# Kernel optimization log

Hardware: AMD Instinct MI355X
Metric: run time of the kernel (lower is better)

Reference implementation:

```python
import jax, jax.numpy as jnp
import numpy as np
import math

E = 768      # embed_size
H = 12       # heads
D = E // H   # head_dim = 64
MAXLEN = 512
N = 8        # batch
L = 512      # seq_len (q_len == k_len)


def _sinusoid_table():
    # (2*MAXLEN-1, E) sinusoidal table, sin at even dims, cos at odd dims
    pos = jnp.arange(2 * MAXLEN - 1, dtype=jnp.float32)[:, None]
    div = jnp.exp(jnp.arange(0, E, 2, dtype=jnp.float32) * (-math.log(10000.0) / E))
    ang = pos * div  # (2M-1, E/2)
    return jnp.stack([jnp.sin(ang), jnp.cos(ang)], axis=-1).reshape(2 * MAXLEN - 1, E)


def setup_inputs() -> dict:
    key = jax.random.key(0)
    ks = jax.random.split(key, 16)
    sc = 0.02
    return {
        "values": jax.random.normal(ks[0], (N, L, E), jnp.float32),
        "keys": jax.random.normal(ks[1], (N, L, E), jnp.float32),
        "query": jax.random.normal(ks[2], (N, L, E), jnp.float32),
        "Wq": jax.random.normal(ks[3], (E, E), jnp.float32) * sc,
        "bq": jax.random.normal(ks[4], (E,), jnp.float32) * sc,
        "Wk": jax.random.normal(ks[5], (E, E), jnp.float32) * sc,
        "bk": jax.random.normal(ks[6], (E,), jnp.float32) * sc,
        "Wv": jax.random.normal(ks[7], (E, E), jnp.float32) * sc,
        "bv": jax.random.normal(ks[8], (E,), jnp.float32) * sc,
        "Wo": jax.random.normal(ks[9], (E, E), jnp.float32) * sc,
        "bo": jax.random.normal(ks[10], (E,), jnp.float32) * sc,
        "Wpos": jax.random.normal(ks[11], (E, E), jnp.float32) * sc,
        "bpos": jax.random.normal(ks[12], (E,), jnp.float32) * sc,
        "r_w_bias": jax.random.normal(ks[13], (H, D), jnp.float32),
        "r_r_bias": jax.random.normal(ks[14], (H, D), jnp.float32),
    }


def _rel_shift(x):
    # Faithful to the torch code: pad one row on q dim, shape-preserving view,
    # drop first row -> identity as written.
    xp = jnp.pad(x, ((0, 0), (0, 0), (1, 0), (0, 0)))
    return xp[:, :, 1:, :]


def reference(values, keys, query, Wq, bq, Wk, bk, Wv, bv, Wo, bo, Wpos, bpos, r_w_bias, r_r_bias):
    pe = _sinusoid_table()  # (2M-1, E)
    r = jnp.arange(L)
    idx = jnp.clip(r[:, None] - r[None, :] + (MAXLEN - 1), 0, 2 * MAXLEN - 2)  # (L, L)
    rel = pe[idx] @ Wpos + bpos                       # (L, L, E)
    rel = rel.reshape(L, L, H, D).transpose(2, 0, 1, 3)  # (H, L, L, D)

    q = (query @ Wq + bq).reshape(N, L, H, D)
    k = (keys @ Wk + bk).reshape(N, L, H, D)
    v = (values @ Wv + bv).reshape(N, L, H, D)

    ac = jnp.einsum('nqhd,nkhd->nhqk', q + r_w_bias[None, None], k)
    bd = jnp.einsum('nqhd,hqkd->nhqk', q + r_r_bias[None, None], rel)
    bd = _rel_shift(bd)

    scores = (ac + bd) / math.sqrt(D)
    attn = jax.nn.softmax(scores, axis=-1)
    out = jnp.einsum('nhqk,nkhd->nqhd', attn, v).reshape(N, L, E)
    return out @ Wo + bo
```

## Files before the change

kernel.cpp:

```cpp
#include <hip/hip_runtime.h>

typedef unsigned short u16;
typedef unsigned int u32;
typedef __bf16 bf16x8 __attribute__((ext_vector_type(8)));
typedef float f32x4 __attribute__((ext_vector_type(4)));

#define EMB 768
#define NH 12
#define HD 64
#define SEQ 512
#define NB 8
#define NLROWS 4096
#define PEROWS 1024

__device__ __forceinline__ float b2f(u16 u) {
    return __uint_as_float(((u32)u) << 16);
}
__device__ __forceinline__ u16 f2b(float f) {
    u32 x = __float_as_uint(f);
    u32 r = x + 0x7fffu + ((x >> 16) & 1u);
    return (u16)(r >> 16);
}
__device__ __forceinline__ u32 pack2(float a, float b) {
    return (u32)f2b(a) | ((u32)f2b(b) << 16);
}
__device__ __forceinline__ void gl_lds16(const u16* g, u16* l) {
    __builtin_amdgcn_global_load_lds((const __attribute__((address_space(1))) u32*)g,
                                     (__attribute__((address_space(3))) u32*)l, 16, 0, 0);
}

__global__ __launch_bounds__(256) void prep(
        const float* __restrict__ Wq, const float* __restrict__ Wk, const float* __restrict__ Wv,
        const float* __restrict__ Wo, const float* __restrict__ Wpos,
        u16* __restrict__ Wt, u16* __restrict__ pe,
        const float* __restrict__ q, const float* __restrict__ k, const float* __restrict__ v,
        u16* __restrict__ qc, u16* __restrict__ kc, u16* __restrict__ vc) {
    __shared__ u16 tile[32][33];
    int b = blockIdx.x;
    int tid = threadIdx.x;
    if (b < 2880) {
        int m = b / 576, r = b % 576;
        const float* src = (m == 0) ? Wq : (m == 1) ? Wk : (m == 2) ? Wv : (m == 3) ? Wo : Wpos;
        u16* dst = Wt + (size_t)m * EMB * EMB;
        int bx = (r % 24) * 32, by = (r / 24) * 32;
        int tx = tid & 31, ty = tid >> 5;
#pragma unroll
        for (int i = 0; i < 32; i += 8)
            tile[ty + i][tx] = f2b(src[(size_t)(by + ty + i) * EMB + bx + tx]);
        __syncthreads();
#pragma unroll
        for (int i = 0; i < 32; i += 8)
            dst[(size_t)(bx + ty + i) * EMB + by + tx] = tile[tx][ty + i];
    } else if (b < 3904) {
        int pos = b - 2880;
        int p2 = pos > 1022 ? 1022 : pos;
#pragma unroll
        for (int j = 0; j < 3; j++) {
            int col = tid + j * 256;
            int i = col >> 1;
            float ang = (float)p2 * __expf(-0.023985261384f * (float)i);
            float val = (col & 1) ? __cosf(ang) : __sinf(ang);
            pe[(size_t)pos * EMB + col] = f2b(val);
        }
    } else {
        int idx = b - 3904;
        int w = idx / 1536, bx = idx % 1536;
        const float* s = (w == 0) ? q : (w == 1) ? k : v;
        u16* d = (w == 0) ? qc : (w == 1) ? kc : vc;
        size_t i = ((size_t)bx * 256 + tid) * 8;
        float4 f0 = *(const float4*)(s + i);
        float4 f1 = *(const float4*)(s + i + 4);
        uint4 o;
        o.x = pack2(f0.x, f0.y); o.y = pack2(f0.z, f0.w);
        o.z = pack2(f1.x, f1.y); o.w = pack2(f1.z, f1.w);
        *(uint4*)(d + i) = o;
    }
}

template <int BM, int BN, int NZ, bool OUTF32>
__global__ __launch_bounds__(256, 4) void gemm_k(
        const u16* A0, const u16* A1, const u16* A2, const u16* A3,
        const u16* W0, const u16* W1, const u16* W2, const u16* W3,
        const float* f0, const float* f1, const float* f2, const float* f3,
        void* C0, void* C1, void* C2, void* C3) {
    constexpr int RT = BM / 32;
    constexpr int CT = BN / 32;
    __shared__ __align__(16) u16 As[BM * 64];
    __shared__ __align__(16) u16 Bs[BN * 64];
    int z = (NZ > 1) ? blockIdx.z : 0;
    if (NZ > 1 && z == 3 && blockIdx.x >= PEROWS / BM) return;
    const u16* A = (z == 0) ? A0 : (z == 1) ? A1 : (z == 2) ? A2 : A3;
    const u16* Bt = (z == 0) ? W0 : (z == 1) ? W1 : (z == 2) ? W2 : W3;
    const float* bias = (z == 0) ? f0 : (z == 1) ? f1 : (z == 2) ? f2 : f3;
    void* Cv = (z == 0) ? C0 : (z == 1) ? C1 : (z == 2) ? C2 : C3;
    bool vtout = (NZ > 1) && (z == 2);

    int tid = threadIdx.x;
    int wave = tid >> 6, lane = tid & 63;
    int lrow = lane & 15, lq = lane >> 4;
    int lr8 = lane >> 3, lb = lane & 7;
    int m0 = blockIdx.x * BM, n0 = blockIdx.y * BN;
    int wr = (wave >> 1) * (BM / 2), wc = (wave & 1) * (BN / 2);
    const u16* Abase = A + (size_t)m0 * EMB + (size_t)(lb ^ lr8) * 8;
    const u16* Bbase = Bt + (size_t)n0 * EMB + (size_t)(lb ^ lr8) * 8;
    f32x4 acc[RT][CT] = {};

    for (int k0 = 0; k0 < EMB; k0 += 64) {
        __syncthreads();
#pragma unroll
        for (int j = 0; j < BM / 32; j++) {
            int row = j * 32 + wave * 8 + lr8;
            gl_lds16(Abase + (size_t)row * EMB + k0, &As[(j * 32 + wave * 8) * 64]);
        }
#pragma unroll
        for (int j = 0; j < BN / 32; j++) {
            int row = j * 32 + wave * 8 + lr8;
            gl_lds16(Bbase + (size_t)row * EMB + k0, &Bs[(j * 32 + wave * 8) * 64]);
        }
        __syncthreads();
#pragma unroll
        for (int ks = 0; ks < 2; ks++) {
            int pb = (ks * 4 + lq) ^ (lrow & 7);
            bf16x8 bfr[CT];
#pragma unroll
            for (int ct = 0; ct < CT; ct++)
                bfr[ct] = *(const bf16x8*)&Bs[(wc + ct * 16 + lrow) * 64 + pb * 8];
#pragma unroll
            for (int rt = 0; rt < RT; rt++) {
                bf16x8 afr = *(const bf16x8*)&As[(wr + rt * 16 + lrow) * 64 + pb * 8];
#pragma unroll
                for (int ct = 0; ct < CT; ct++)
                    acc[rt][ct] = __builtin_amdgcn_mfma_f32_16x16x32_bf16(afr, bfr[ct], acc[rt][ct], 0, 0, 0);
            }
        }
    }
#pragma unroll
    for (int rt = 0; rt < RT; rt++) {
#pragma unroll
        for (int ct = 0; ct < CT; ct++) {
            int col = n0 + wc + ct * 16 + lrow;
            float bvv = bias[col];
            int mrow = m0 + wr + rt * 16 + lq * 4;
            if (vtout) {
                int nb = mrow >> 9, kvl = mrow & 511;
                int hh = col >> 6, dl = col & 63;
                ushort4 pk;
                pk.x = f2b(acc[rt][ct][0] + bvv);
                pk.y = f2b(acc[rt][ct][1] + bvv);
                pk.z = f2b(acc[rt][ct][2] + bvv);
                pk.w = f2b(acc[rt][ct][3] + bvv);
                *(ushort4*)((u16*)Cv + (((size_t)(nb * NH + hh) * HD + dl) << 9) + kvl) = pk;
            } else if (OUTF32) {
#pragma unroll
                for (int r = 0; r < 4; r++)
                    ((float*)Cv)[(size_t)(mrow + r) * EMB + col] = acc[rt][ct][r] + bvv;
            } else {
#pragma unroll
                for (int r = 0; r < 4; r++)
                    ((u16*)Cv)[(size_t)(mrow + r) * EMB + col] = f2b(acc[rt][ct][r] + bvv);
            }
        }
    }
}

__global__ __launch_bounds__(256, 3) void attn_rpe(
        const u16* __restrict__ Qb, const u16* __restrict__ Kb, const u16* __restrict__ Vtg,
        const u16* __restrict__ Rb, const float* __restrict__ rwb, const float* __restrict__ rrb,
        u16* __restrict__ Ctx) {
    __shared__ __align__(16) u16 Ks[64 * 64];
    __shared__ __align__(16) u16 Vt[64 * 64];
    __shared__ __align__(16) u16 Rs[128 * 64];
    __shared__ __align__(16) u16 PsPb[4 * 1664];

    int q0 = blockIdx.x * 64;
    int h = blockIdx.y;
    int n = blockIdx.z;
    int tid = threadIdx.x;
    int wave = tid >> 6, lane = tid & 63;
    int lrow = lane & 15, lq = lane >> 4;
    int lr8 = lane >> 3, lb = lane & 7;
    int swz = (lb ^ lr8) * 8;
    u16* psd = &PsPb[wave * 1664];

    bf16x8 aw[2], ar[2];
    {
        const u16* qrow = Qb + ((size_t)(n * SEQ + q0 + wave * 16 + lrow)) * EMB + h * HD;
#pragma unroll
        for (int ks = 0; ks < 2; ks++) {
            int c = ks * 32 + lq * 8;
            uint4 qv = *(const uint4*)(qrow + c);
            float4 w0 = *(const float4*)(rwb + h * HD + c);
            float4 w1 = *(const float4*)(rwb + h * HD + c + 4);
            float4 r0 = *(const float4*)(rrb + h * HD + c);
            float4 r1 = *(const float4*)(rrb + h * HD + c + 4);
            union { uint4 u; u16 s[8]; } qu; qu.u = qv;
            union { uint4 u; bf16x8 v; } ww, rr;
            ww.u.x = pack2(b2f(qu.s[0]) + w0.x, b2f(qu.s[1]) + w0.y);
            ww.u.y = pack2(b2f(qu.s[2]) + w0.z, b2f(qu.s[3]) + w0.w);
            ww.u.z = pack2(b2f(qu.s[4]) + w1.x, b2f(qu.s[5]) + w1.y);
            ww.u.w = pack2(b2f(qu.s[6]) + w1.z, b2f(qu.s[7]) + w1.w);
            rr.u.x = pack2(b2f(qu.s[0]) + r0.x, b2f(qu.s[1]) + r0.y);
            rr.u.y = pack2(b2f(qu.s[2]) + r0.z, b2f(qu.s[3]) + r0.w);
            rr.u.z = pack2(b2f(qu.s[4]) + r1.x, b2f(qu.s[5]) + r1.y);
            rr.u.w = pack2(b2f(qu.s[6]) + r1.z, b2f(qu.s[7]) + r1.w);
            aw[ks] = ww.v;
            ar[ks] = rr.v;
        }
    }

    auto stage_chunk = [&](int cc) {
#pragma unroll
        for (int j = 0; j < 2; j++) {
            int row = j * 32 + wave * 8 + lr8;
            gl_lds16(Kb + ((size_t)(n * SEQ + cc + row)) * EMB + h * HD + swz,
                     &Ks[(j * 32 + wave * 8) * 64]);
        }
#pragma unroll
        for (int j = 0; j < 2; j++) {
            int row = j * 32 + wave * 8 + lr8;
            gl_lds16(Vtg + (((size_t)(n * NH + h) * HD + row) << 9) + cc + swz,
                     &Vt[(j * 32 + wave * 8) * 64]);
        }
#pragma unroll
        for (int j = 0; j < 4; j++) {
            int row = j * 32 + wave * 8 + lr8;
            gl_lds16(Rb + (size_t)(q0 - cc + 448 + row) * EMB + h * HD + swz,
                     &Rs[(j * 32 + wave * 8) * 64]);
        }
    };

    float ls[4] = {0.f, 0.f, 0.f, 0.f};
    f32x4 acco[4] = {};

    stage_chunk(0);
    for (int c0 = 0; c0 < SEQ; c0 += 64) {
        __syncthreads();

        f32x4 sacc[4] = {};
        f32x4 pacc[5] = {};
        bf16x8 vf[2][4];
#pragma unroll
        for (int ks = 0; ks < 2; ks++) {
            int pb = (ks * 4 + lq) ^ (lrow & 7);
#pragma unroll
            for (int ct = 0; ct < 4; ct++) {
                bf16x8 bk = *(const bf16x8*)&Ks[(ct * 16 + lrow) * 64 + pb * 8];
                sacc[ct] = __builtin_amdgcn_mfma_f32_16x16x32_bf16(aw[ks], bk, sacc[ct], 0, 0, 0);
            }
#pragma unroll
            for (int jj = 0; jj < 5; jj++) {
                bf16x8 br = *(const bf16x8*)&Rs[((wave + jj) * 16 + lrow) * 64 + pb * 8];
                pacc[jj] = __builtin_amdgcn_mfma_f32_16x16x32_bf16(ar[ks], br, pacc[jj], 0, 0, 0);
            }
#pragma unroll
            for (int dt = 0; dt < 4; dt++)
                vf[ks][dt] = *(const bf16x8*)&Vt[(dt * 16 + lrow) * 64 + pb * 8];
        }
        __syncthreads();
        if (c0 + 64 < SEQ) stage_chunk(c0 + 64);

#pragma unroll
        for (int jj = 0; jj < 5; jj++) {
            ushort4 pk;
            pk.x = f2b(pacc[jj][0]); pk.y = f2b(pacc[jj][1]);
            pk.z = f2b(pacc[jj][2]); pk.w = f2b(pacc[jj][3]);
            *(ushort4*)&psd[(jj * 16 + lrow) * 20 + lq * 4] = pk;
        }

        float bd[4][4];
#pragma unroll
        for (int ct = 0; ct < 4; ct++)
#pragma unroll
            for (int r = 0; r < 4; r++) {
                int jwin = lq * 4 + r - (ct * 16 + lrow) + 63;
                bd[ct][r] = b2f(psd[jwin * 20 + lq * 4 + r]);
            }
#pragma unroll
        for (int ct = 0; ct < 4; ct++)
#pragma unroll
            for (int r = 0; r < 4; r++) {
                float p = exp2f((sacc[ct][r] + bd[ct][r]) * 0.18033688011f);
                ls[r] += p;
                psd[(lq * 4 + r) * 72 + ct * 16 + lrow] = f2b(p);
            }

#pragma unroll
        for (int ks = 0; ks < 2; ks++) {
            bf16x8 pf = *(const bf16x8*)&psd[lrow * 72 + ks * 32 + lq * 8];
#pragma unroll
            for (int dt = 0; dt < 4; dt++)
                acco[dt] = __builtin_amdgcn_mfma_f32_16x16x32_bf16(vf[ks][dt], pf, acco[dt], 0, 0, 0);
        }
    }

#pragma unroll
    for (int r = 0; r < 4; r++) {
#pragma unroll
        for (int msk = 1; msk < 16; msk <<= 1)
            ls[r] += __shfl_xor(ls[r], msk);
    }
    float* lsb = (float*)Rs;
    if (lrow == 0) {
#pragma unroll
        for (int r = 0; r < 4; r++)
            lsb[wave * 16 + lq * 4 + r] = ls[r];
    }
    float inv = 1.0f / lsb[wave * 16 + lrow];
    int q = q0 + wave * 16 + lrow;
#pragma unroll
    for (int dt = 0; dt < 4; dt++) {
        ushort4 pk;
        pk.x = f2b(acco[dt][0] * inv);
        pk.y = f2b(acco[dt][1] * inv);
        pk.z = f2b(acco[dt][2] * inv);
        pk.w = f2b(acco[dt][3] * inv);
        *(ushort4*)&Ctx[((size_t)(n * SEQ + q)) * EMB + h * HD + dt * 16 + lq * 4] = pk;
    }
}

extern "C" void kernel_launch(void* const* d_in, const int* in_sizes, int n_in,
                              void* d_out, int out_size, void* d_ws, size_t ws_size,
                              hipStream_t stream) {
    const float* values = (const float*)d_in[0];
    const float* keys   = (const float*)d_in[1];
    const float* query  = (const float*)d_in[2];
    const float* Wq = (const float*)d_in[3];
    const float* bq = (const float*)d_in[4];
    const float* Wk = (const float*)d_in[5];
    const float* bk = (const float*)d_in[6];
    const float* Wv = (const float*)d_in[7];
    const float* bv = (const float*)d_in[8];
    const float* Wo = (const float*)d_in[9];
    const float* bo = (const float*)d_in[10];
    const float* Wpos = (const float*)d_in[11];
    const float* bpos = (const float*)d_in[12];
    const float* rwb = (const float*)d_in[13];
    const float* rrb = (const float*)d_in[14];
    float* out = (float*)d_out;

    u16* ws = (u16*)d_ws;
    size_t off = 0;
    u16* Wt = ws;            off += (size_t)5 * EMB * EMB;
    u16* pe = ws + off;      off += (size_t)PEROWS * EMB;
    u16* Rb = ws + off;      off += (size_t)PEROWS * EMB;
    u16* qc = ws + off;      off += (size_t)NLROWS * EMB;
    u16* kc = ws + off;      off += (size_t)NLROWS * EMB;
    u16* vc = ws + off;      off += (size_t)NLROWS * EMB;
    u16* Qp = ws + off;      off += (size_t)NLROWS * EMB;
    u16* Kp = ws + off;      off += (size_t)NLROWS * EMB;
    u16* Vtg = ws + off;     off += (size_t)NLROWS * EMB;
    u16* Cx = qc;

    prep<<<dim3(8512), dim3(256), 0, stream>>>(Wq, Wk, Wv, Wo, Wpos, Wt, pe,
                                               query, keys, values, qc, kc, vc);

    gemm_k<128, 96, 4, false><<<dim3(32, 8, 4), dim3(256), 0, stream>>>(
        qc, kc, vc, pe,
        Wt, Wt + (size_t)1 * EMB * EMB, Wt + (size_t)2 * EMB * EMB, Wt + (size_t)4 * EMB * EMB,
        bq, bk, bv, bpos,
        Qp, Kp, Vtg, Rb);

    attn_rpe<<<dim3(8, NH, NB), dim3(256), 0, stream>>>(Qp, Kp, Vtg, Rb, rwb, rrb, Cx);

    gemm_k<64, 96, 1, true><<<dim3(64, 8), dim3(256), 0, stream>>>(
        Cx, Cx, Cx, Cx,
        Wt + (size_t)3 * EMB * EMB, Wt + (size_t)3 * EMB * EMB,
        Wt + (size_t)3 * EMB * EMB, Wt + (size_t)3 * EMB * EMB,
        bo, bo, bo, bo,
        out, out, out, out);
}
```

Before: 179.3 us.

## Load K, V and R fragments directly from global memory instead of LDS staging

The attention kernel no longer stages K, transposed V and relative-position tiles into shared memory with async global-to-LDS loads and block barriers. Each wave now reads its MFMA operand fragments straight from global memory, relying on L1/L2 caching. This removes the per-chunk __syncthreads and shared-memory traffic and frees LDS for higher occupancy. The cost is redundant global loads across waves (K and V are reread by all four waves), no prefetch overlap with compute, and exposed load latency.

```diff
diff --git a/kernel.cpp b/kernel.cpp
--- a/kernel.cpp
+++ b/kernel.cpp
@@ -23,6 +23,9 @@
 }
 __device__ __forceinline__ u32 pack2(float a, float b) {
     return (u32)f2b(a) | ((u32)f2b(b) << 16);
+}
+__device__ __forceinline__ bf16x8 ld16(const u16* p) {
+    return *(const bf16x8*)p;
 }
 __device__ __forceinline__ void gl_lds16(const u16* g, u16* l) {
     __builtin_amdgcn_global_load_lds((const __attribute__((address_space(1))) u32*)g,
@@ -167,10 +170,8 @@
         const u16* __restrict__ Qb, const u16* __restrict__ Kb, const u16* __restrict__ Vtg,
         const u16* __restrict__ Rb, const float* __restrict__ rwb, const float* __restrict__ rrb,
         u16* __restrict__ Ctx) {
-    __shared__ __align__(16) u16 Ks[64 * 64];
-    __shared__ __align__(16) u16 Vt[64 * 64];
-    __shared__ __align__(16) u16 Rs[128 * 64];
     __shared__ __align__(16) u16 PsPb[4 * 1664];
+    __shared__ float lsb[64];
 
     int q0 = blockIdx.x * 64;
     int h = blockIdx.y;
@@ -178,8 +179,6 @@
     int tid = threadIdx.x;
     int wave = tid >> 6, lane = tid & 63;
     int lrow = lane & 15, lq = lane >> 4;
-    int lr8 = lane >> 3, lb = lane & 7;
-    int swz = (lb ^ lr8) * 8;
     u16* psd = &PsPb[wave * 1664];
 
     bf16x8 aw[2], ar[2];
@@ -208,56 +207,38 @@
         }
     }
 
-    auto stage_chunk = [&](int cc) {
-#pragma unroll
-        for (int j = 0; j < 2; j++) {
-            int row = j * 32 + wave * 8 + lr8;
-            gl_lds16(Kb + ((size_t)(n * SEQ + cc + row)) * EMB + h * HD + swz,
-                     &Ks[(j * 32 + wave * 8) * 64]);
-        }
-#pragma unroll
-        for (int j = 0; j < 2; j++) {
-            int row = j * 32 + wave * 8 + lr8;
-            gl_lds16(Vtg + (((size_t)(n * NH + h) * HD + row) << 9) + cc + swz,
-                     &Vt[(j * 32 + wave * 8) * 64]);
-        }
-#pragma unroll
-        for (int j = 0; j < 4; j++) {
-            int row = j * 32 + wave * 8 + lr8;
-            gl_lds16(Rb + (size_t)(q0 - cc + 448 + row) * EMB + h * HD + swz,
-                     &Rs[(j * 32 + wave * 8) * 64]);
-        }
-    };
-
     float ls[4] = {0.f, 0.f, 0.f, 0.f};
     f32x4 acco[4] = {};
 
-    stage_chunk(0);
     for (int c0 = 0; c0 < SEQ; c0 += 64) {
-        __syncthreads();
+        const u16* kbase = Kb + ((size_t)(n * SEQ + c0)) * EMB + h * HD;
+        const u16* vbase = Vtg + (((size_t)(n * NH + h) * HD) << 9) + c0;
+        const u16* rbase = Rb + (size_t)(q0 - c0 + 448) * EMB + h * HD;
 
         f32x4 sacc[4] = {};
         f32x4 pacc[5] = {};
         bf16x8 vf[2][4];
 #pragma unroll
         for (int ks = 0; ks < 2; ks++) {
-            int pb = (ks * 4 + lq) ^ (lrow & 7);
-#pragma unroll
-            for (int ct = 0; ct < 4; ct++) {
-                bf16x8 bk = *(const bf16x8*)&Ks[(ct * 16 + lrow) * 64 + pb * 8];
-                sacc[ct] = __builtin_amdgcn_mfma_f32_16x16x32_bf16(aw[ks], bk, sacc[ct], 0, 0, 0);
-            }
-#pragma unroll
-            for (int jj = 0; jj < 5; jj++) {
-                bf16x8 br = *(const bf16x8*)&Rs[((wave + jj) * 16 + lrow) * 64 + pb * 8];
-                pacc[jj] = __builtin_amdgcn_mfma_f32_16x16x32_bf16(ar[ks], br, pacc[jj], 0, 0, 0);
-            }
+            int koff = ks * 32 + lq * 8;
+            bf16x8 bk[4];
+#pragma unroll
+            for (int ct = 0; ct < 4; ct++)
+                bk[ct] = ld16(kbase + (size_t)(ct * 16 + lrow) * EMB + koff);
+            bf16x8 br[5];
+#pragma unroll
+            for (int jj = 0; jj < 5; jj++)
+                br[jj] = ld16(rbase + (size_t)((wave + jj) * 16 + lrow) * EMB + koff);
 #pragma unroll
             for (int dt = 0; dt < 4; dt++)
-                vf[ks][dt] = *(const bf16x8*)&Vt[(dt * 16 + lrow) * 64 + pb * 8];
-        }
-        __syncthreads();
-        if (c0 + 64 < SEQ) stage_chunk(c0 + 64);
+                vf[ks][dt] = ld16(vbase + ((size_t)(dt * 16 + lrow) << 9) + koff);
+#pragma unroll
+            for (int ct = 0; ct < 4; ct++)
+                sacc[ct] = __builtin_amdgcn_mfma_f32_16x16x32_bf16(aw[ks], bk[ct], sacc[ct], 0, 0, 0);
+#pragma unroll
+            for (int jj = 0; jj < 5; jj++)
+                pacc[jj] = __builtin_amdgcn_mfma_f32_16x16x32_bf16(ar[ks], br[jj], pacc[jj], 0, 0, 0);
+        }
 
 #pragma unroll
         for (int jj = 0; jj < 5; jj++) {
@@ -299,7 +280,6 @@
         for (int msk = 1; msk < 16; msk <<= 1)
             ls[r] += __shfl_xor(ls[r], msk);
     }
-    float* lsb = (float*)Rs;
     if (lrow == 0) {
 #pragma unroll
         for (int r = 0; r < 4; r++)
```

Result: slower. 230.5 us (+28.5%).
